# Optimization experiments

Measured on AMD Instinct MI355X. Metric: run time of the kernel, lower is better.

The kernel has to match this reference:

```python
import jax, jax.numpy as jnp
import numpy as np

# --- hash-grid / Field hyperparams (from init_kwargs defaults) ---
L = 16            # n_levels
F = 2             # n_features_per_level
LOG2_T = 19
T = 1 << LOG2_T   # hashmap size per level
NMIN = 16         # base_resolution
MAXRES = 512
SCALE = 1.0
HIDDEN = 32
OUT_DIM = 1
N = 2_000_000
B = float(np.exp(np.log(MAXRES * SCALE / NMIN) / (L - 1)))  # per_level_scale
PRIMES = jnp.array([1, 2654435761, 805459861], dtype=jnp.uint32)
# 8 corner offsets of the unit cube, (8,3)
CORNERS = jnp.array([[(c >> 0) & 1, (c >> 1) & 1, (c >> 2) & 1] for c in range(8)], dtype=jnp.uint32)


def hash_encode(xn, table):
    """xn: (N,3) in [0,1]; table: (L,T,F). Returns (N, L*F)."""
    feats = []
    for l in range(L):  # fixed small loop over levels
        s = NMIN * (B ** l) - 1.0          # tcnn-style grid scale
        pos = xn * s                        # (N,3)
        p0 = jnp.floor(pos)
        w = pos - p0                        # trilinear fracs, (N,3)
        p0i = p0.astype(jnp.uint32)
        corner = p0i[:, None, :] + CORNERS[None, :, :]          # (N,8,3)
        h = corner * PRIMES                                      # (N,8,3) uint32 wrap-mul
        idx = (h[..., 0] ^ h[..., 1] ^ h[..., 2]) & jnp.uint32(T - 1)  # (N,8)
        # trilinear weights per corner: prod over dims of w or (1-w)
        cw = jnp.where(CORNERS[None, :, :] == 1, w[:, None, :], 1.0 - w[:, None, :])
        cw = cw.prod(axis=-1)                                    # (N,8)
        g = table[l][idx.astype(jnp.int32)]                      # (N,8,F)
        feats.append(jnp.einsum('ncf,nc->nf', g, cw))            # (N,F)
    return jnp.concatenate(feats, axis=-1)                       # (N, L*F)


def setup_inputs() -> dict:
    key = jax.random.key(0)
    ks = jax.random.split(key, 8)
    x = jax.random.uniform(ks[0], (N, 3), jnp.float32)  # coords in [0,1) subset of [-scale,scale]
    table = jax.random.normal(ks[1], (L, T, F), jnp.float32) * 1e-2
    W0 = jax.random.normal(ks[2], (L * F + 3, HIDDEN), jnp.float32) * 0.1
    b0 = jnp.zeros((HIDDEN,), jnp.float32)
    W1 = jax.random.normal(ks[3], (HIDDEN, HIDDEN), jnp.float32) * 0.1
    b1 = jnp.zeros((HIDDEN,), jnp.float32)
    Wout = jax.random.normal(ks[4], (HIDDEN, OUT_DIM), jnp.float32) * 0.1
    bout = jnp.zeros((OUT_DIM,), jnp.float32)
    return {"x": x, "table": table, "W0": W0, "b0": b0, "W1": W1, "b1": b1, "Wout": Wout, "bout": bout}


def reference(x, table, W0, b0, W1, b1, Wout, bout):
    # density(): normalize coords to [0,1]
    xn = (x + SCALE) / (2.0 * SCALE)
    # back_prop=0: encoder sees detached coords
    h = hash_encode(jax.lax.stop_gradient(xn), table)   # (N, L*F)
    feat = jnp.concatenate([xn, h], axis=-1)            # (N, 35)  torch.cat([x, h], 1)
    h1 = jax.nn.elu(feat @ W0 + b0)
    h2 = jax.nn.elu(h1 @ W1 + b1)
    out = h2 @ Wout + bout                              # (N, 1)
    return out
```

## Files before the change

### kernel.cpp

```cpp
#include <hip/hip_runtime.h>
#include <hip/hip_fp16.h>
#include <cmath>

#define LVL   16
#define NDENSE 11
#define NHASH  (LVL - NDENSE)
#define TSIZE (1u << 19)
#define TMASK (TSIZE - 1u)
#define HID   32
#define PRIME1 2654435761u
#define PRIME2 805459861u
#define FSTRIDE 72

struct Scales { float s[LVL]; };
struct DenseInfo {
    int X0[NDENSE];
    int dim[NDENSE];
    int dimsq[NDENSE];
    int base[NDENSE];
    int eoff[NDENSE + 1];
};

typedef _Float16 f16x8 __attribute__((ext_vector_type(8)));
typedef float    f32x4 __attribute__((ext_vector_type(4)));
typedef float    f32x2 __attribute__((ext_vector_type(2)));
typedef unsigned u32x4 __attribute__((ext_vector_type(4)));

__device__ __forceinline__ float elu_f(float v) {
    return v > 0.0f ? v : expm1f(v);
}
__device__ __forceinline__ unsigned sel4(u32x4 v, unsigned s) {
    unsigned lo = (s & 1) ? v.y : v.x;
    unsigned hi = (s & 1) ? v.w : v.z;
    return (s & 2) ? hi : lo;
}
__device__ __forceinline__ unsigned hashed(unsigned cx, unsigned cy, unsigned cz) {
    return (cx ^ (cy * PRIME1) ^ (cz * PRIME2)) & TMASK;
}

__device__ __forceinline__ unsigned enc8(float v) {
    unsigned short t = __half_as_ushort(__float2half_rn(v * 0.0625f));
    unsigned m = (unsigned)(t & 0x7FFF) + 0x40u;
    return ((t >> 8) & 0x80u) | (m >> 7);
}
__device__ __forceinline__ float2 dec2(unsigned hw) {
    unsigned h2 = ((hw & 0x8000u) << 16) | ((hw & 0x7F00u) << 15)
                | ((hw & 0x80u)   << 8)  | ((hw & 0x7Fu)   << 7);
    __half2 hh; __builtin_memcpy(&hh, &h2, 4);
    return __half22float2(hh);
}

__global__ __launch_bounds__(256)
void convert_hash8(const f32x2* __restrict__ src, unsigned short* __restrict__ dst)
{
    int i = blockIdx.x * blockDim.x + threadIdx.x;
    if (i >= NHASH * (int)TSIZE) return;
    int l = NDENSE + i / (int)TSIZE;
    int s = i & (int)TMASK;
    f32x2 v = src[(size_t)l * TSIZE + s];
    dst[i] = (unsigned short)(enc8(v.x) | (enc8(v.y) << 8));
}

__global__ __launch_bounds__(256)
void dense_prep8(const float* __restrict__ table, u32x4* __restrict__ dtab,
                 DenseInfo di)
{
    int e = blockIdx.x * blockDim.x + threadIdx.x;
    if (e >= di.eoff[NDENSE]) return;
    int l = 0;
#pragma unroll
    for (int k = 1; k < NDENSE; ++k) if (e >= di.eoff[k]) l = k;
    int le = e - di.eoff[l];
    int D = di.dim[l];
    int ex = le % D; int r = le / D;
    int ey = r % D;  int ez = r / D;
    unsigned cx = (unsigned)(di.X0[l] + ex);
    unsigned cy = (unsigned)(di.X0[l] + ey);
    unsigned cz = (unsigned)(di.X0[l] + ez);
    const f32x2* __restrict__ tl = (const f32x2*)table + (size_t)l * TSIZE;
    f32x2 c0 = tl[hashed(cx,      cy,      cz)];
    f32x2 c1 = tl[hashed(cx + 1u, cy,      cz)];
    f32x2 c2 = tl[hashed(cx,      cy + 1u, cz)];
    f32x2 c3 = tl[hashed(cx + 1u, cy + 1u, cz)];
    f32x2 c4 = tl[hashed(cx,      cy,      cz + 1u)];
    f32x2 c5 = tl[hashed(cx + 1u, cy,      cz + 1u)];
    f32x2 c6 = tl[hashed(cx,      cy + 1u, cz + 1u)];
    f32x2 c7 = tl[hashed(cx + 1u, cy + 1u, cz + 1u)];
    u32x4 q;
    q.x = enc8(c0.x) | (enc8(c0.y) << 8) | (enc8(c1.x) << 16) | (enc8(c1.y) << 24);
    q.y = enc8(c2.x) | (enc8(c2.y) << 8) | (enc8(c3.x) << 16) | (enc8(c3.y) << 24);
    q.z = enc8(c4.x) | (enc8(c4.y) << 8) | (enc8(c5.x) << 16) | (enc8(c5.y) << 24);
    q.w = enc8(c6.x) | (enc8(c6.y) << 8) | (enc8(c7.x) << 16) | (enc8(c7.y) << 24);
    dtab[di.base[l] + le] = q;
}

__global__ void prep_frags(const float* __restrict__ W0, const float* __restrict__ W1,
                           const float* __restrict__ Wout, _Float16* __restrict__ frags)
{
    int idx = blockIdx.x * blockDim.x + threadIdx.x;
    if (idx >= 14*64*8) return;
    int f = idx >> 9;
    int rem = idx & 511;
    int lane = rem >> 3;
    int j = rem & 7;
    int q = lane >> 4;
    int nn = lane & 15;

    float w = 0.0f;
    bool lo;
    if (f < 8) {
        int part = f >> 2, kt = (f >> 1) & 1, nt = f & 1;
        int k = kt*32 + q*8 + j;
        int ncol = nt*16 + nn;
        float val = 0.0f;
        if (k < 32)      val = W0[(3 + k)  * HID + ncol];
        else if (k < 35) val = W0[(k - 32) * HID + ncol];
        else if (k < 38) val = W0[(k - 35) * HID + ncol];
        w = val; lo = (part == 1);
    } else if (f < 12) {
        int part = (f - 8) >> 1, nt = (f - 8) & 1;
        int k = q*8 + j;
        int ncol = nt*16 + nn;
        w = W1[k * HID + ncol]; lo = (part == 1);
    } else {
        int part = f - 12;
        int k = q*8 + j;
        w = (nn == 0) ? Wout[k] : 0.0f; lo = (part == 1);
    }
    _Float16 hi = (_Float16)w;
    frags[idx] = lo ? (_Float16)(w - (float)hi) : hi;
}

__global__ __launch_bounds__(256, 4)
void fused_mfma_kernel(const float* __restrict__ x, const u32x4* __restrict__ htab8,
                       const u32x4* __restrict__ dtab,
                       const float* __restrict__ b0, const float* __restrict__ b1,
                       const float* __restrict__ bout, const _Float16* __restrict__ fragbuf,
                       float* __restrict__ out, int n, Scales sc, DenseInfo di)
{
    __shared__ __attribute__((aligned(16))) _Float16 featL[256 * FSTRIDE];
    __shared__ __attribute__((aligned(16))) _Float16 h1h[4][16*32], h1l[4][16*32];
    __shared__ __attribute__((aligned(16))) _Float16 h2h[4][16*32], h2l[4][16*32];

    const int t = threadIdx.x;
    const int pbase = blockIdx.x * 256;
    const int p  = pbase + t;
    const int pc = p < n ? p : n - 1;

    const float xn0 = (x[3*pc+0] + 1.0f) * 0.5f;
    const float xn1 = (x[3*pc+1] + 1.0f) * 0.5f;
    const float xn2 = (x[3*pc+2] + 1.0f) * 0.5f;

    _Float16* row = &featL[t * FSTRIDE];
    {
        _Float16 h0 = (_Float16)xn0, h1_ = (_Float16)xn1, h2_ = (_Float16)xn2;
        row[32] = h0; row[33] = h1_; row[34] = h2_;
        row[35] = (_Float16)(xn0 - (float)h0);
        row[36] = (_Float16)(xn1 - (float)h1_);
        row[37] = (_Float16)(xn2 - (float)h2_);
#pragma unroll
        for (int k = 38; k < 64; ++k) row[k] = (_Float16)0.0f;
    }

#pragma unroll
    for (int l = 0; l < NDENSE; ++l) {
        const float s = sc.s[l];
        float px = xn0 * s, py = xn1 * s, pz = xn2 * s;
        float fx = floorf(px), fy = floorf(py), fz = floorf(pz);
        float wx = px - fx, wy = py - fy, wz = pz - fz;
        int D = di.dim[l], Dsq = di.dimsq[l], X0 = di.X0[l];
        int cx = (int)fx - X0, cy = (int)fy - X0, cz = (int)fz - X0;
        cx = min(max(cx, 0), D - 1);
        cy = min(max(cy, 0), D - 1);
        cz = min(max(cz, 0), D - 1);
        u32x4 Q = dtab[(size_t)(di.base[l] + cx + cy * D + cz * Dsq)];
        float2 a00 = dec2(Q.x & 0xFFFFu), a10 = dec2(Q.x >> 16);
        float2 a01 = dec2(Q.y & 0xFFFFu), a11 = dec2(Q.y >> 16);
        float2 c00 = dec2(Q.z & 0xFFFFu), c10 = dec2(Q.z >> 16);
        float2 c01 = dec2(Q.w & 0xFFFFu), c11 = dec2(Q.w >> 16);
        float ux = 1.0f - wx, uy = 1.0f - wy, uz = 1.0f - wz;
        float b0x = uy*(ux*a00.x + wx*a10.x) + wy*(ux*a01.x + wx*a11.x);
        float b0y = uy*(ux*a00.y + wx*a10.y) + wy*(ux*a01.y + wx*a11.y);
        float b1x = uy*(ux*c00.x + wx*c10.x) + wy*(ux*c01.x + wx*c11.x);
        float b1y = uy*(ux*c00.y + wx*c10.y) + wy*(ux*c01.y + wx*c11.y);
        row[2*l + 0] = (_Float16)(16.0f * (uz * b0x + wz * b1x));
        row[2*l + 1] = (_Float16)(16.0f * (uz * b0y + wz * b1y));
    }

#pragma unroll
    for (int l = NDENSE; l < LVL; ++l) {
        const u32x4* __restrict__ qt = htab8 + ((size_t)(l - NDENSE) * TSIZE >> 3);
        const float s = sc.s[l];
        float px = xn0 * s, py = xn1 * s, pz = xn2 * s;
        float fx = floorf(px), fy = floorf(py), fz = floorf(pz);
        float wx = px - fx, wy = py - fy, wz = pz - fz;
        unsigned x0 = (unsigned)fx, y0 = (unsigned)fy, z0 = (unsigned)fz;
        unsigned hy0 = y0 * PRIME1, hy1 = hy0 + PRIME1;
        unsigned hz0 = z0 * PRIME2, hz1 = hz0 + PRIME2;
        unsigned b00 = hy0 ^ hz0, b10 = hy1 ^ hz0, b01 = hy0 ^ hz1, b11 = hy1 ^ hz1;
        unsigned i0 = (x0 ^ b00) & TMASK;
        unsigned i1 = (x0 ^ b10) & TMASK;
        unsigned i2 = (x0 ^ b01) & TMASK;
        unsigned i3 = (x0 ^ b11) & TMASK;

        u32x4 Q0 = qt[i0 >> 3];
        u32x4 Q1 = qt[i1 >> 3];
        u32x4 Q2 = qt[i2 >> 3];
        u32x4 Q3 = qt[i3 >> 3];

        unsigned dm = (x0 ^ (x0 + 1u)) & TMASK;
        unsigned j0 = i0 ^ dm, j1 = i1 ^ dm, j2 = i2 ^ dm, j3 = i3 ^ dm;

        unsigned hc0, hc1, hc2, hc3;
        if ((x0 & 7u) == 7u) {
            u32x4 R0 = qt[j0 >> 3];
            u32x4 R1 = qt[j1 >> 3];
            u32x4 R2 = qt[j2 >> 3];
            u32x4 R3 = qt[j3 >> 3];
            unsigned d0 = sel4(R0, (j0 >> 1) & 3), d1 = sel4(R1, (j1 >> 1) & 3);
            unsigned d2 = sel4(R2, (j2 >> 1) & 3), d3 = sel4(R3, (j3 >> 1) & 3);
            hc0 = (j0 & 1) ? (d0 >> 16) : (d0 & 0xFFFFu);
            hc1 = (j1 & 1) ? (d1 >> 16) : (d1 & 0xFFFFu);
            hc2 = (j2 & 1) ? (d2 >> 16) : (d2 & 0xFFFFu);
            hc3 = (j3 & 1) ? (d3 >> 16) : (d3 & 0xFFFFu);
        } else {
            unsigned d0 = sel4(Q0, (j0 >> 1) & 3), d1 = sel4(Q1, (j1 >> 1) & 3);
            unsigned d2 = sel4(Q2, (j2 >> 1) & 3), d3 = sel4(Q3, (j3 >> 1) & 3);
            hc0 = (j0 & 1) ? (d0 >> 16) : (d0 & 0xFFFFu);
            hc1 = (j1 & 1) ? (d1 >> 16) : (d1 & 0xFFFFu);
            hc2 = (j2 & 1) ? (d2 >> 16) : (d2 & 0xFFFFu);
            hc3 = (j3 & 1) ? (d3 >> 16) : (d3 & 0xFFFFu);
        }
        unsigned e0 = sel4(Q0, (i0 >> 1) & 3), e1 = sel4(Q1, (i1 >> 1) & 3);
        unsigned e2 = sel4(Q2, (i2 >> 1) & 3), e3 = sel4(Q3, (i3 >> 1) & 3);
        unsigned ha0 = (i0 & 1) ? (e0 >> 16) : (e0 & 0xFFFFu);
        unsigned ha1 = (i1 & 1) ? (e1 >> 16) : (e1 & 0xFFFFu);
        unsigned ha2 = (i2 & 1) ? (e2 >> 16) : (e2 & 0xFFFFu);
        unsigned ha3 = (i3 & 1) ? (e3 >> 16) : (e3 & 0xFFFFu);

        float2 A0 = dec2(ha0), A1 = dec2(ha1), A2 = dec2(ha2), A3 = dec2(ha3);
        float2 C0 = dec2(hc0), C1 = dec2(hc1), C2 = dec2(hc2), C3 = dec2(hc3);
        float ux = 1.0f - wx, uy = 1.0f - wy, uz = 1.0f - wz;
        float w00 = uy*uz, w10 = wy*uz, w01 = uy*wz, w11 = wy*wz;
        float f0 = ux * (w00*A0.x + w10*A1.x + w01*A2.x + w11*A3.x)
                 + wx * (w00*C0.x + w10*C1.x + w01*C2.x + w11*C3.x);
        float f1 = ux * (w00*A0.y + w10*A1.y + w01*A2.y + w11*A3.y)
                 + wx * (w00*C0.y + w10*C1.y + w01*C2.y + w11*C3.y);

        row[2*l + 0] = (_Float16)(16.0f * f0);
        row[2*l + 1] = (_Float16)(16.0f * f1);
    }
    __syncthreads();

    const int l = t & 63, w = t >> 6;
    const int q = l >> 4, nn = l & 15;

    const f16x8* FB = (const f16x8*)fragbuf;
    f16x8 B0h00 = FB[0*64 + l], B0h01 = FB[1*64 + l];
    f16x8 B0h10 = FB[2*64 + l], B0h11 = FB[3*64 + l];
    f16x8 B0l00 = FB[4*64 + l], B0l01 = FB[5*64 + l];
    f16x8 B0l10 = FB[6*64 + l], B0l11 = FB[7*64 + l];
    f16x8 B1h0  = FB[8*64 + l], B1h1  = FB[9*64 + l];
    f16x8 B1l0  = FB[10*64 + l], B1l1 = FB[11*64 + l];
    f16x8 B2h   = FB[12*64 + l], B2l  = FB[13*64 + l];

    float bias00 = b0[nn], bias01 = b0[16 + nn];
    float bias10 = b1[nn], bias11 = b1[16 + nn];
    float biasO  = (nn == 0) ? bout[0] : 0.0f;

    _Float16* H1h = &h1h[w][0]; _Float16* H1l = &h1l[w][0];
    _Float16* H2h = &h2h[w][0]; _Float16* H2l = &h2l[w][0];

#pragma unroll
    for (int mt = 0; mt < 4; ++mt) {
        const int mrow = w*64 + mt*16 + nn;
        const _Float16* arow = &featL[mrow * FSTRIDE];

        f16x8 A0 = *(const f16x8*)(arow + q*8);
        f16x8 A1 = *(const f16x8*)(arow + 32 + q*8);
        f32x4 c0 = {bias00, bias00, bias00, bias00};
        f32x4 c1 = {bias01, bias01, bias01, bias01};
        c0 = __builtin_amdgcn_mfma_f32_16x16x32_f16(A0, B0h00, c0, 0, 0, 0);
        c0 = __builtin_amdgcn_mfma_f32_16x16x32_f16(A1, B0h10, c0, 0, 0, 0);
        c0 = __builtin_amdgcn_mfma_f32_16x16x32_f16(A0, B0l00, c0, 0, 0, 0);
        c0 = __builtin_amdgcn_mfma_f32_16x16x32_f16(A1, B0l10, c0, 0, 0, 0);
        c1 = __builtin_amdgcn_mfma_f32_16x16x32_f16(A0, B0h01, c1, 0, 0, 0);
        c1 = __builtin_amdgcn_mfma_f32_16x16x32_f16(A1, B0h11, c1, 0, 0, 0);
        c1 = __builtin_amdgcn_mfma_f32_16x16x32_f16(A0, B0l01, c1, 0, 0, 0);
        c1 = __builtin_amdgcn_mfma_f32_16x16x32_f16(A1, B0l11, c1, 0, 0, 0);

#pragma unroll
        for (int r = 0; r < 4; ++r) {
            int m = q*4 + r;
            float e0 = elu_f(c0[r]);
            _Float16 hh = (_Float16)e0;
            H1h[m*32 + nn]      = hh;
            H1l[m*32 + nn]      = (_Float16)(e0 - (float)hh);
            float e1 = elu_f(c1[r]);
            hh = (_Float16)e1;
            H1h[m*32 + 16 + nn] = hh;
            H1l[m*32 + 16 + nn] = (_Float16)(e1 - (float)hh);
        }

        f16x8 Ah = *(const f16x8*)(H1h + nn*32 + q*8);
        f16x8 Al = *(const f16x8*)(H1l + nn*32 + q*8);
        f32x4 d0 = {bias10, bias10, bias10, bias10};
        f32x4 d1 = {bias11, bias11, bias11, bias11};
        d0 = __builtin_amdgcn_mfma_f32_16x16x32_f16(Ah, B1h0, d0, 0, 0, 0);
        d0 = __builtin_amdgcn_mfma_f32_16x16x32_f16(Ah, B1l0, d0, 0, 0, 0);
        d0 = __builtin_amdgcn_mfma_f32_16x16x32_f16(Al, B1h0, d0, 0, 0, 0);
        d1 = __builtin_amdgcn_mfma_f32_16x16x32_f16(Ah, B1h1, d1, 0, 0, 0);
        d1 = __builtin_amdgcn_mfma_f32_16x16x32_f16(Ah, B1l1, d1, 0, 0, 0);
        d1 = __builtin_amdgcn_mfma_f32_16x16x32_f16(Al, B1h1, d1, 0, 0, 0);

#pragma unroll
        for (int r = 0; r < 4; ++r) {
            int m = q*4 + r;
            float e0 = elu_f(d0[r]);
            _Float16 hh = (_Float16)e0;
            H2h[m*32 + nn]      = hh;
            H2l[m*32 + nn]      = (_Float16)(e0 - (float)hh);
            float e1 = elu_f(d1[r]);
            hh = (_Float16)e1;
            H2h[m*32 + 16 + nn] = hh;
            H2l[m*32 + 16 + nn] = (_Float16)(e1 - (float)hh);
        }

        f16x8 A2h = *(const f16x8*)(H2h + nn*32 + q*8);
        f16x8 A2l = *(const f16x8*)(H2l + nn*32 + q*8);
        f32x4 c3 = {biasO, biasO, biasO, biasO};
        c3 = __builtin_amdgcn_mfma_f32_16x16x32_f16(A2h, B2h, c3, 0, 0, 0);
        c3 = __builtin_amdgcn_mfma_f32_16x16x32_f16(A2h, B2l, c3, 0, 0, 0);
        c3 = __builtin_amdgcn_mfma_f32_16x16x32_f16(A2l, B2h, c3, 0, 0, 0);

        if (nn == 0) {
            int pout = pbase + w*64 + mt*16 + q*4;
#pragma unroll
            for (int r = 0; r < 4; ++r)
                if (pout + r < n) out[pout + r] = c3[r];
        }
    }
}

__device__ __forceinline__ float2 enc_level_f32(float xn0, float xn1, float xn2, float s,
                                                const float2* __restrict__ tb)
{
    float px = xn0 * s, py = xn1 * s, pz = xn2 * s;
    float fx = floorf(px), fy = floorf(py), fz = floorf(pz);
    float wx = px - fx, wy = py - fy, wz = pz - fz;
    unsigned x0 = (unsigned)fx, y0 = (unsigned)fy, z0 = (unsigned)fz;
    unsigned hy0 = y0 * PRIME1, hy1 = hy0 + PRIME1;
    unsigned hz0 = z0 * PRIME2, hz1 = hz0 + PRIME2;
    unsigned b00 = hy0 ^ hz0, b10 = hy1 ^ hz0, b01 = hy0 ^ hz1, b11 = hy1 ^ hz1;
    float2 g000 = tb[( x0       ^ b00) & TMASK];
    float2 g100 = tb[((x0 + 1u) ^ b00) & TMASK];
    float2 g010 = tb[( x0       ^ b10) & TMASK];
    float2 g110 = tb[((x0 + 1u) ^ b10) & TMASK];
    float2 g001 = tb[( x0       ^ b01) & TMASK];
    float2 g101 = tb[((x0 + 1u) ^ b01) & TMASK];
    float2 g011 = tb[( x0       ^ b11) & TMASK];
    float2 g111 = tb[((x0 + 1u) ^ b11) & TMASK];
    float ux = 1.0f - wx, uy = 1.0f - wy, uz = 1.0f - wz;
    float c00 = uy*uz, c10 = wy*uz, c01 = uy*wz, c11 = wy*wz;
    float f0 = ux * (c00*g000.x + c10*g010.x + c01*g001.x + c11*g011.x)
             + wx * (c00*g100.x + c10*g110.x + c01*g101.x + c11*g111.x);
    float f1 = ux * (c00*g000.y + c10*g010.y + c01*g001.y + c11*g011.y)
             + wx * (c00*g100.y + c10*g110.y + c01*g101.y + c11*g111.y);
    return make_float2(f0, f1);
}

__global__ __launch_bounds__(256, 4)
void fused_fp32_kernel(const float* __restrict__ x, const float* __restrict__ table,
                       const float* __restrict__ W0, const float* __restrict__ b0,
                       const float* __restrict__ W1, const float* __restrict__ b1,
                       const float* __restrict__ Wout, const float* __restrict__ bout,
                       float* __restrict__ out, int n, Scales sc)
{
    int tid = blockIdx.x * blockDim.x + threadIdx.x;
    if (tid >= n) return;
    float xn0 = (x[3*tid+0] + 1.0f) * 0.5f;
    float xn1 = (x[3*tid+1] + 1.0f) * 0.5f;
    float xn2 = (x[3*tid+2] + 1.0f) * 0.5f;
    float acc[HID];
#pragma unroll
    for (int j = 0; j < HID; ++j)
        acc[j] = b0[j] + xn0 * W0[0*HID + j] + xn1 * W0[1*HID + j] + xn2 * W0[2*HID + j];
#pragma unroll
    for (int lv = 0; lv < LVL; ++lv) {
        const float2* tb = (const float2*)table + (size_t)lv * TSIZE;
        float2 f = enc_level_f32(xn0, xn1, xn2, sc.s[lv], tb);
        const float* w0r0 = W0 + (3 + 2*lv) * HID;
        const float* w0r1 = W0 + (4 + 2*lv) * HID;
#pragma unroll
        for (int j = 0; j < HID; ++j)
            acc[j] += f.x * w0r0[j] + f.y * w0r1[j];
    }
#pragma unroll
    for (int j = 0; j < HID; ++j) acc[j] = elu_f(acc[j]);
    float acc2[HID];
#pragma unroll
    for (int j = 0; j < HID; ++j) acc2[j] = b1[j];
#pragma unroll
    for (int k = 0; k < HID; ++k) {
        float hk = acc[k];
        const float* w1r = W1 + k * HID;
#pragma unroll
        for (int j = 0; j < HID; ++j) acc2[j] += hk * w1r[j];
    }
    float o = bout[0];
#pragma unroll
    for (int k = 0; k < HID; ++k) o += elu_f(acc2[k]) * Wout[k];
    out[tid] = o;
}

extern "C" void kernel_launch(void* const* d_in, const int* in_sizes, int n_in,
                              void* d_out, int out_size, void* d_ws, size_t ws_size,
                              hipStream_t stream)
{
    const float* x    = (const float*)d_in[0];
    const float* tb   = (const float*)d_in[1];
    const float* W0   = (const float*)d_in[2];
    const float* b0   = (const float*)d_in[3];
    const float* W1   = (const float*)d_in[4];
    const float* b1   = (const float*)d_in[5];
    const float* Wout = (const float*)d_in[6];
    const float* bo   = (const float*)d_in[7];
    float* out = (float*)d_out;

    int n = in_sizes[0] / 3;

    Scales sc;
    DenseInfo di;
    double B = exp(log(32.0) / 15.0);
    {
        int base = 0, ecum = 0;
        for (int l = 0; l < LVL; ++l) {
            double sd = 16.0 * pow(B, (double)l) - 1.0;
            sc.s[l] = (float)sd;
            if (l < NDENSE) {
                int X0   = (int)floor(0.5 * sd) - 2; if (X0 < 0) X0 = 0;
                int Xmax = (int)ceil(sd) + 2;
                int dim  = Xmax - X0 + 1;
                di.X0[l] = X0; di.dim[l] = dim; di.dimsq[l] = dim * dim;
                di.base[l] = base; di.eoff[l] = ecum;
                base += dim * dim * dim;
                ecum += dim * dim * dim;
            }
        }
        di.eoff[NDENSE] = ecum;
    }

    const size_t dense_bytes = (size_t)di.eoff[NDENSE] * 16;
    const size_t hash8_bytes = (size_t)NHASH * TSIZE * 2;
    const size_t frag_bytes  = 14 * 64 * 8 * sizeof(_Float16);
    int block = 256;
    int pgrid = (n + block - 1) / block;

    if (ws_size >= dense_bytes + hash8_bytes + frag_bytes) {
        u32x4*          dtab  = (u32x4*)d_ws;
        unsigned short* htab8 = (unsigned short*)((char*)d_ws + dense_bytes);
        _Float16*       frags = (_Float16*)((char*)d_ws + dense_bytes + hash8_bytes);
        int hgrid = (NHASH * (int)TSIZE + block - 1) / block;
        convert_hash8<<<hgrid, block, 0, stream>>>((const f32x2*)tb, htab8);
        int dgrid = (di.eoff[NDENSE] + block - 1) / block;
        dense_prep8<<<dgrid, block, 0, stream>>>(tb, dtab, di);
        prep_frags<<<28, 256, 0, stream>>>(W0, W1, Wout, frags);
        fused_mfma_kernel<<<pgrid, block, 0, stream>>>(x, (const u32x4*)htab8, dtab,
                                                       b0, b1, bo, frags, out, n, sc, di);
    } else {
        fused_fp32_kernel<<<pgrid, block, 0, stream>>>(x, tb, W0, b0, W1, b1, Wout, bo, out, n, sc);
    }
}
```

Measured before the change: 522.7 us.

## Swizzle feature rows in LDS, drop block barrier, reuse hidden buffers

```diff
diff --git a/kernel.cpp b/kernel.cpp
--- a/kernel.cpp
+++ b/kernel.cpp
@@ -10,7 +10,6 @@
 #define HID   32
 #define PRIME1 2654435761u
 #define PRIME2 805459861u
-#define FSTRIDE 72
 
 struct Scales { float s[LVL]; };
 struct DenseInfo {
@@ -27,7 +26,7 @@
 typedef unsigned u32x4 __attribute__((ext_vector_type(4)));
 
 __device__ __forceinline__ float elu_f(float v) {
-    return v > 0.0f ? v : expm1f(v);
+    return v > 0.0f ? v : __expf(v) - 1.0f;
 }
 __device__ __forceinline__ unsigned sel4(u32x4 v, unsigned s) {
     unsigned lo = (s & 1) ? v.y : v.x;
@@ -48,6 +47,11 @@
                 | ((hw & 0x80u)   << 8)  | ((hw & 0x7Fu)   << 7);
     __half2 hh; __builtin_memcpy(&hh, &h2, 4);
     return __half22float2(hh);
+}
+__device__ __forceinline__ unsigned pack_ff(_Float16 a, _Float16 b) {
+    unsigned short ua = __builtin_bit_cast(unsigned short, a);
+    unsigned short ub = __builtin_bit_cast(unsigned short, b);
+    return (unsigned)ua | ((unsigned)ub << 16);
 }
 
 __global__ __launch_bounds__(256)
@@ -138,9 +142,8 @@
                        const float* __restrict__ bout, const _Float16* __restrict__ fragbuf,
                        float* __restrict__ out, int n, Scales sc, DenseInfo di)
 {
-    __shared__ __attribute__((aligned(16))) _Float16 featL[256 * FSTRIDE];
+    __shared__ __attribute__((aligned(16))) _Float16 featL[256 * 64];
     __shared__ __attribute__((aligned(16))) _Float16 h1h[4][16*32], h1l[4][16*32];
-    __shared__ __attribute__((aligned(16))) _Float16 h2h[4][16*32], h2l[4][16*32];
 
     const int t = threadIdx.x;
     const int pbase = blockIdx.x * 256;
@@ -151,15 +154,21 @@
     const float xn1 = (x[3*pc+1] + 1.0f) * 0.5f;
     const float xn2 = (x[3*pc+2] + 1.0f) * 0.5f;
 
-    _Float16* row = &featL[t * FSTRIDE];
+    unsigned* __restrict__ rowd = (unsigned*)&featL[t * 64];
+    const int swt = t & 7;
+
     {
-        _Float16 h0 = (_Float16)xn0, h1_ = (_Float16)xn1, h2_ = (_Float16)xn2;
-        row[32] = h0; row[33] = h1_; row[34] = h2_;
-        row[35] = (_Float16)(xn0 - (float)h0);
-        row[36] = (_Float16)(xn1 - (float)h1_);
-        row[37] = (_Float16)(xn2 - (float)h2_);
-#pragma unroll
-        for (int k = 38; k < 64; ++k) row[k] = (_Float16)0.0f;
+        u32x4* fl = (u32x4*)rowd;
+        _Float16 X0h = (_Float16)xn0, X1h = (_Float16)xn1, X2h = (_Float16)xn2;
+        _Float16 L0h = (_Float16)(xn0 - (float)X0h);
+        _Float16 L1h = (_Float16)(xn1 - (float)X1h);
+        _Float16 L2h = (_Float16)(xn2 - (float)X2h);
+        u32x4 ch;
+        ch.x = pack_ff(X0h, X1h); ch.y = pack_ff(X2h, L0h);
+        ch.z = pack_ff(L1h, L2h); ch.w = 0;
+        fl[4 ^ swt] = ch;
+        u32x4 Z; Z.x = 0; Z.y = 0; Z.z = 0; Z.w = 0;
+        fl[5 ^ swt] = Z; fl[6 ^ swt] = Z; fl[7 ^ swt] = Z;
     }
 
 #pragma unroll
@@ -183,8 +192,9 @@
         float b0y = uy*(ux*a00.y + wx*a10.y) + wy*(ux*a01.y + wx*a11.y);
         float b1x = uy*(ux*c00.x + wx*c10.x) + wy*(ux*c01.x + wx*c11.x);
         float b1y = uy*(ux*c00.y + wx*c10.y) + wy*(ux*c01.y + wx*c11.y);
-        row[2*l + 0] = (_Float16)(16.0f * (uz * b0x + wz * b1x));
-        row[2*l + 1] = (_Float16)(16.0f * (uz * b0y + wz * b1y));
+        _Float16 f0 = (_Float16)(16.0f * (uz * b0x + wz * b1x));
+        _Float16 f1 = (_Float16)(16.0f * (uz * b0y + wz * b1y));
+        rowd[(((l >> 2) ^ swt) << 2) + (l & 3)] = pack_ff(f0, f1);
     }
 
 #pragma unroll
@@ -247,37 +257,35 @@
         float f1 = ux * (w00*A0.y + w10*A1.y + w01*A2.y + w11*A3.y)
                  + wx * (w00*C0.y + w10*C1.y + w01*C2.y + w11*C3.y);
 
-        row[2*l + 0] = (_Float16)(16.0f * f0);
-        row[2*l + 1] = (_Float16)(16.0f * f1);
-    }
-    __syncthreads();
-
-    const int l = t & 63, w = t >> 6;
-    const int q = l >> 4, nn = l & 15;
+        rowd[(((l >> 2) ^ swt) << 2) + (l & 3)] =
+            pack_ff((_Float16)(16.0f * f0), (_Float16)(16.0f * f1));
+    }
+
+    const int lane = t & 63, w = t >> 6;
+    const int q = lane >> 4, nn = lane & 15;
 
     const f16x8* FB = (const f16x8*)fragbuf;
-    f16x8 B0h00 = FB[0*64 + l], B0h01 = FB[1*64 + l];
-    f16x8 B0h10 = FB[2*64 + l], B0h11 = FB[3*64 + l];
-    f16x8 B0l00 = FB[4*64 + l], B0l01 = FB[5*64 + l];
-    f16x8 B0l10 = FB[6*64 + l], B0l11 = FB[7*64 + l];
-    f16x8 B1h0  = FB[8*64 + l], B1h1  = FB[9*64 + l];
-    f16x8 B1l0  = FB[10*64 + l], B1l1 = FB[11*64 + l];
-    f16x8 B2h   = FB[12*64 + l], B2l  = FB[13*64 + l];
+    f16x8 B0h00 = FB[0*64 + lane], B0h01 = FB[1*64 + lane];
+    f16x8 B0h10 = FB[2*64 + lane], B0h11 = FB[3*64 + lane];
+    f16x8 B0l00 = FB[4*64 + lane], B0l01 = FB[5*64 + lane];
+    f16x8 B0l10 = FB[6*64 + lane], B0l11 = FB[7*64 + lane];
+    f16x8 B1h0  = FB[8*64 + lane], B1h1  = FB[9*64 + lane];
+    f16x8 B1l0  = FB[10*64 + lane], B1l1 = FB[11*64 + lane];
+    f16x8 B2h   = FB[12*64 + lane], B2l  = FB[13*64 + lane];
 
     float bias00 = b0[nn], bias01 = b0[16 + nn];
     float bias10 = b1[nn], bias11 = b1[16 + nn];
     float biasO  = (nn == 0) ? bout[0] : 0.0f;
 
     _Float16* H1h = &h1h[w][0]; _Float16* H1l = &h1l[w][0];
-    _Float16* H2h = &h2h[w][0]; _Float16* H2l = &h2l[w][0];
 
 #pragma unroll
     for (int mt = 0; mt < 4; ++mt) {
         const int mrow = w*64 + mt*16 + nn;
-        const _Float16* arow = &featL[mrow * FSTRIDE];
-
-        f16x8 A0 = *(const f16x8*)(arow + q*8);
-        f16x8 A1 = *(const f16x8*)(arow + 32 + q*8);
+        const f16x8* ar = (const f16x8*)&featL[mrow * 64];
+        f16x8 A0 = ar[q ^ (nn & 7)];
+        f16x8 A1 = ar[(4 + q) ^ (nn & 7)];
+
         f32x4 c0 = {bias00, bias00, bias00, bias00};
         f32x4 c1 = {bias01, bias01, bias01, bias01};
         c0 = __builtin_amdgcn_mfma_f32_16x16x32_f16(A0, B0h00, c0, 0, 0, 0);
@@ -318,16 +326,16 @@
             int m = q*4 + r;
             float e0 = elu_f(d0[r]);
             _Float16 hh = (_Float16)e0;
-            H2h[m*32 + nn]      = hh;
-            H2l[m*32 + nn]      = (_Float16)(e0 - (float)hh);
+            H1h[m*32 + nn]      = hh;
+            H1l[m*32 + nn]      = (_Float16)(e0 - (float)hh);
             float e1 = elu_f(d1[r]);
             hh = (_Float16)e1;
-            H2h[m*32 + 16 + nn] = hh;
-            H2l[m*32 + 16 + nn] = (_Float16)(e1 - (float)hh);
+            H1h[m*32 + 16 + nn] = hh;
+            H1l[m*32 + 16 + nn] = (_Float16)(e1 - (float)hh);
         }
 
-        f16x8 A2h = *(const f16x8*)(H2h + nn*32 + q*8);
-        f16x8 A2l = *(const f16x8*)(H2l + nn*32 + q*8);
+        f16x8 A2h = *(const f16x8*)(H1h + nn*32 + q*8);
+        f16x8 A2l = *(const f16x8*)(H1l + nn*32 + q*8);
         f32x4 c3 = {biasO, biasO, biasO, biasO};
         c3 = __builtin_amdgcn_mfma_f32_16x16x32_f16(A2h, B2h, c3, 0, 0, 0);
         c3 = __builtin_amdgcn_mfma_f32_16x16x32_f16(A2h, B2l, c3, 0, 0, 0);
```

Result: no change. 516.4 us (-1.2%).
